# Kernel optimization log

Hardware: AMD Instinct MI355X
Metric: run time of the kernel (lower is better)

Reference implementation:

```python
import jax, jax.numpy as jnp
import numpy as np

# Module hyperparameters (init_kwargs)
N_CLASSES = 21
RADIUS = 5
SIZE = (256, 256)
SIGMA_DIST = 4.0
SIGMA_FEAT = 1.0
B, C = 8, 32


def _offsets(radius):
    """Integer (dy, dx) offsets with Euclidean distance < radius (includes (0,0))."""
    offs = []
    r = int(radius)
    for dy in range(-r + 1, r):
        for dx in range(-r + 1, r):
            if dy * dy + dx * dx < radius * radius:
                offs.append((dy, dx))
    return offs


OFFSETS = _offsets(RADIUS)  # 69 offsets for radius=5


def setup_inputs() -> dict:
    key = jax.random.key(0)
    k1, k2 = jax.random.split(key)
    H, W = SIZE
    classification = jax.random.uniform(k1, (B, N_CLASSES, H, W), dtype=jnp.float32)
    features = jax.random.normal(k2, (B, C, H, W), dtype=jnp.float32)
    return {"classification": classification, "features": features}


def reference(classification, features):
    # classification: [B, K, H, W] soft assignments S
    # features:       [B, C, H, W]
    Bb, K, H, W = classification.shape
    inv_sd2 = 1.0 / (SIGMA_DIST * SIGMA_DIST)
    inv_sf2 = 1.0 / (SIGMA_FEAT * SIGMA_FEAT)

    hs = jnp.arange(H)
    ws = jnp.arange(W)

    WS = jnp.zeros_like(classification)           # (W @ S), [B, K, H, W]
    degree = jnp.zeros((Bb, H, W), classification.dtype)

    # Loop over the small fixed set of neighbor offsets (69 for radius=5).
    for dy, dx in OFFSETS:
        f_nb = jnp.roll(features, (-dy, -dx), axis=(2, 3))
        s_nb = jnp.roll(classification, (-dy, -dx), axis=(2, 3))
        # mask out wrap-around: neighbor (h+dy, w+dx) must be in-bounds
        valid_h = (hs + dy >= 0) & (hs + dy < H)
        valid_w = (ws + dx >= 0) & (ws + dx < W)
        mask = (valid_h[:, None] & valid_w[None, :]).astype(classification.dtype)
        # Gaussian affinity: distance kernel * feature kernel
        feat_d2 = ((features - f_nb) ** 2).sum(axis=1)        # [B, H, W]
        w = jnp.exp(-(dy * dy + dx * dx) * inv_sd2 - feat_d2 * inv_sf2) * mask
        WS = WS + w[:, None] * s_nb
        degree = degree + w

    # numerator   = S^T W S : [B, K, K]
    # denominator = d^T S   : [B, K]
    num = jnp.einsum('bkhw,bjhw->bkj', classification, WS)
    den = jnp.einsum('bhw,bkhw->bk', degree, classification)
    return (num / den[:, None, :]).sum()
```

## Files before the change

kernel.cpp:

```cpp
#include <hip/hip_runtime.h>

#define HH 256
#define WW 256
#define HWPX 65536
#define BB 8
#define KK 21
#define CC 32

typedef _Float16 half2v __attribute__((ext_vector_type(2)));
union F4H { float4 f4; half2v h[4]; };

__global__ __launch_bounds__(256) void prep(const float* __restrict__ cls,
                                            const float* __restrict__ feat,
                                            float4* __restrict__ fpk,
                                            float2* __restrict__ TN) {
    const int tid = blockIdx.x * 256 + threadIdx.x;
    const int p4 = tid * 4;
    const int b = p4 >> 16;
    const int p = p4 & (HWPX - 1);

    const float* cbase = cls + (size_t)b * KK * HWPX + p;
    float4 s = make_float4(0.f, 0.f, 0.f, 0.f);
#pragma unroll
    for (int k = 0; k < KK; ++k) {
        float4 c = *(const float4*)(cbase + (size_t)k * HWPX);
        s.x += c.x; s.y += c.y; s.z += c.z; s.w += c.w;
    }

    const float* src = feat + (size_t)b * CC * HWPX + p;
    float nq[4] = {0.f, 0.f, 0.f, 0.f};
#pragma unroll
    for (int j = 0; j < 4; ++j) {
        float4 ch[8];
#pragma unroll
        for (int c = 0; c < 8; ++c)
            ch[c] = *(const float4*)(src + (size_t)(j * 8 + c) * HWPX);
#pragma unroll
        for (int px = 0; px < 4; ++px) {
            F4H u;
#pragma unroll
            for (int k = 0; k < 4; ++k) {
                float a  = ((const float*)&ch[2 * k])[px];
                float b2 = ((const float*)&ch[2 * k + 1])[px];
                u.h[k] = __builtin_bit_cast(half2v, __builtin_amdgcn_cvt_pkrtz(a, b2));
                nq[px] = __builtin_amdgcn_fdot2(u.h[k], u.h[k], nq[px], false);
            }
            fpk[(size_t)j * (BB * HWPX) + p4 + px] = u.f4;
        }
    }
    const float* sa = (const float*)&s;
#pragma unroll
    for (int px = 0; px < 4; ++px) TN[p4 + px] = make_float2(sa[px], nq[px]);
}

__global__ __launch_bounds__(256) void affinity4(const float4* __restrict__ fpk,
                                                 const float2* __restrict__ TN,
                                                 float* __restrict__ V,
                                                 float* __restrict__ deg) {
    const int L  = blockIdx.x;
    const int b  = L & 7;
    const int t  = L >> 3;
    const int by = t & 15;
    const int bx = t >> 4;
    const int lane = threadIdx.x & 63;
    const int wid  = threadIdx.x >> 6;
    const int gx  = bx * 64 + lane;
    const int gy0 = by * 16 + wid * 4;

    const size_t bofs = (size_t)b * HWPX;
    const float4* fb0 = fpk + bofs;
    const float4* fb1 = fpk + (size_t)1 * BB * HWPX + bofs;
    const float4* fb2 = fpk + (size_t)2 * BB * HWPX + bofs;
    const float4* fb3 = fpk + (size_t)3 * BB * HWPX + bofs;
    const float2* tnb = TN + bofs;

    F4H fp[4][4];
    float np_[4];
#pragma unroll
    for (int py = 0; py < 4; ++py) {
        const int pp = ((gy0 + py) << 8) | gx;
        fp[py][0].f4 = fb0[pp];
        fp[py][1].f4 = fb1[pp];
        fp[py][2].f4 = fb2[pp];
        fp[py][3].f4 = fb3[pp];
        np_[py] = tnb[pp].y;
    }

    float degacc[4] = {0.f, 0.f, 0.f, 0.f};
    float vacc[4]   = {0.f, 0.f, 0.f, 0.f};

#pragma unroll 1
    for (int dyi = 0; dyi < 12; ++dyi) {
        const int ny = gy0 + dyi - 4;
        if ((unsigned)ny >= HH) continue;
        const int rowq = ny << 8;

        int dy2[4];
        float base[4];
#pragma unroll
        for (int py = 0; py < 4; ++py) {
            const int d = dyi - 4 - py;
            dy2[py] = d * d;
            base[py] = fmaf(-0.03125f, (float)dy2[py], -0.5f * np_[py]);
        }
        const int mind = min(min(dy2[0], dy2[1]), min(dy2[2], dy2[3]));

#pragma unroll 3
        for (int dxi = 0; dxi < 9; ++dxi) {
            const int dx = dxi - 4;
            const int dx2 = dx * dx;
            if (mind + dx2 >= 25) continue;

            const int gx2 = gx + dx;
            const bool vx = (unsigned)gx2 < WW;
            const int q = rowq | min(max(gx2, 0), WW - 1);

            F4H nb0, nb1, nb2, nb3;
            nb0.f4 = fb0[q];
            nb1.f4 = fb1[q];
            nb2.f4 = fb2[q];
            nb3.f4 = fb3[q];
            const float2 tq = tnb[q];
            const float cdx = (float)dx2 * -0.03125f;

#pragma unroll
            for (int py = 0; py < 4; ++py) {
                if (dy2[py] + dx2 < 25) {
                    float acc = fmaf(-0.5f, tq.y, base[py] + cdx);
#pragma unroll
                    for (int k = 0; k < 4; ++k) {
                        acc = __builtin_amdgcn_fdot2(fp[py][0].h[k], nb0.h[k], acc, false);
                        acc = __builtin_amdgcn_fdot2(fp[py][1].h[k], nb1.h[k], acc, false);
                        acc = __builtin_amdgcn_fdot2(fp[py][2].h[k], nb2.h[k], acc, false);
                        acc = __builtin_amdgcn_fdot2(fp[py][3].h[k], nb3.h[k], acc, false);
                    }
                    float w = __builtin_exp2f(acc * 2.8853900817779268f);
                    w = vx ? w : 0.f;
                    degacc[py] += w;
                    vacc[py] = fmaf(w, tq.x, vacc[py]);
                }
            }
        }
    }

#pragma unroll
    for (int py = 0; py < 4; ++py) {
        const size_t o = bofs + ((size_t)(gy0 + py) << 8) + gx;
        V[o] = vacc[py];
        deg[o] = degacc[py];
    }
}

__global__ __launch_bounds__(256) void reduce_bj(const float* __restrict__ cls,
                                                 const float* __restrict__ V,
                                                 const float* __restrict__ deg,
                                                 float* __restrict__ numer,
                                                 float* __restrict__ denom) {
    __shared__ float smN[4][22], smD[4][22];
    const int b = blockIdx.y;
    const int p4 = (blockIdx.x * 256 + threadIdx.x) * 4;

    const float* clsb = cls + (size_t)b * KK * HWPX;
    const float4 v4 = *(const float4*)(V + (size_t)b * HWPX + p4);
    const float4 d4 = *(const float4*)(deg + (size_t)b * HWPX + p4);

    float accN[KK], accD[KK];
#pragma unroll
    for (int j = 0; j < KK; ++j) {
        float4 s4 = *(const float4*)(clsb + (size_t)j * HWPX + p4);
        float n = s4.x * v4.x;  n = fmaf(s4.y, v4.y, n);
        n = fmaf(s4.z, v4.z, n); n = fmaf(s4.w, v4.w, n);
        float d = s4.x * d4.x;  d = fmaf(s4.y, d4.y, d);
        d = fmaf(s4.z, d4.z, d); d = fmaf(s4.w, d4.w, d);
        accN[j] = n; accD[j] = d;
    }

    const int wid = threadIdx.x >> 6;
#pragma unroll
    for (int j = 0; j < KK; ++j) {
        float n = accN[j], d = accD[j];
#pragma unroll
        for (int off = 32; off > 0; off >>= 1) {
            n += __shfl_down(n, off);
            d += __shfl_down(d, off);
        }
        if ((threadIdx.x & 63) == 0) { smN[wid][j] = n; smD[wid][j] = d; }
    }
    __syncthreads();
    if (threadIdx.x < 2 * KK) {
        int half = threadIdx.x / KK;
        int j = threadIdx.x - half * KK;
        float acc = half ? (smD[0][j] + smD[1][j] + smD[2][j] + smD[3][j])
                         : (smN[0][j] + smN[1][j] + smN[2][j] + smN[3][j]);
        float* dst = half ? denom : numer;
        atomicAdd(&dst[b * KK + j], acc);
    }
}

__global__ __launch_bounds__(256) void finalize(const float* __restrict__ numer,
                                                const float* __restrict__ denom,
                                                float* __restrict__ out) {
    __shared__ float sm[4];
    int i = threadIdx.x;
    float r = 0.f;
    if (i < BB * KK) r = numer[i] / denom[i];
#pragma unroll
    for (int off = 32; off > 0; off >>= 1) r += __shfl_down(r, off);
    if ((i & 63) == 0) sm[i >> 6] = r;
    __syncthreads();
    if (i == 0) out[0] = sm[0] + sm[1] + sm[2] + sm[3];
}

extern "C" void kernel_launch(void* const* d_in, const int* in_sizes, int n_in,
                              void* d_out, int out_size, void* d_ws, size_t ws_size,
                              hipStream_t stream) {
    const float* cls  = (const float*)d_in[0];
    const float* feat = (const float*)d_in[1];
    float* out = (float*)d_out;

    const size_t BHW = (size_t)BB * HWPX;
    float4* fpk  = (float4*)d_ws;
    float2* TN   = (float2*)((char*)d_ws + BHW * 64);
    float*  V    = (float*)((char*)TN + BHW * 8);
    float*  deg  = V + BHW;
    float*  numer = deg + BHW;
    float*  denom = numer + BB * KK;

    (void)hipMemsetAsync(numer, 0, 2 * BB * KK * sizeof(float), stream);
    prep<<<dim3(BHW / 1024), dim3(256), 0, stream>>>(cls, feat, fpk, TN);
    affinity4<<<dim3(512), dim3(256), 0, stream>>>(fpk, TN, V, deg);
    reduce_bj<<<dim3(HWPX / 1024, BB), dim3(256), 0, stream>>>(cls, V, deg, numer, denom);
    finalize<<<dim3(1), dim3(256), 0, stream>>>(numer, denom, out);
}
```

Before: 205.9 us.

## Fuse per-class reduction into affinity kernel and halve pixels per prep thread

The affinity kernel now stages its per-pixel V and degree values in shared memory and immediately performs the class-weighted reduction with atomics. This removes the separate reduce kernel and the global round trip of V and degree. The prep kernel processes two pixels per thread instead of four and no longer unrolls the channel-group loop, which cuts register pressure and raises thread count. The cost is extra shared memory and a block-wide sync in the affinity kernel, plus classification reads now happening inside it.

```diff
diff --git a/kernel.cpp b/kernel.cpp
--- a/kernel.cpp
+++ b/kernel.cpp
@@ -15,48 +15,49 @@
                                             float4* __restrict__ fpk,
                                             float2* __restrict__ TN) {
     const int tid = blockIdx.x * 256 + threadIdx.x;
-    const int p4 = tid * 4;
-    const int b = p4 >> 16;
-    const int p = p4 & (HWPX - 1);
+    const int p2 = tid * 2;
+    const int b = p2 >> 16;
+    const int p = p2 & (HWPX - 1);
 
     const float* cbase = cls + (size_t)b * KK * HWPX + p;
-    float4 s = make_float4(0.f, 0.f, 0.f, 0.f);
+    float sx = 0.f, sy = 0.f;
 #pragma unroll
     for (int k = 0; k < KK; ++k) {
-        float4 c = *(const float4*)(cbase + (size_t)k * HWPX);
-        s.x += c.x; s.y += c.y; s.z += c.z; s.w += c.w;
+        float2 c = *(const float2*)(cbase + (size_t)k * HWPX);
+        sx += c.x; sy += c.y;
     }
 
     const float* src = feat + (size_t)b * CC * HWPX + p;
-    float nq[4] = {0.f, 0.f, 0.f, 0.f};
-#pragma unroll
+    float nq0 = 0.f, nq1 = 0.f;
+#pragma unroll 1
     for (int j = 0; j < 4; ++j) {
-        float4 ch[8];
+        float2 ch[8];
 #pragma unroll
         for (int c = 0; c < 8; ++c)
-            ch[c] = *(const float4*)(src + (size_t)(j * 8 + c) * HWPX);
-#pragma unroll
-        for (int px = 0; px < 4; ++px) {
-            F4H u;
-#pragma unroll
-            for (int k = 0; k < 4; ++k) {
-                float a  = ((const float*)&ch[2 * k])[px];
-                float b2 = ((const float*)&ch[2 * k + 1])[px];
-                u.h[k] = __builtin_bit_cast(half2v, __builtin_amdgcn_cvt_pkrtz(a, b2));
-                nq[px] = __builtin_amdgcn_fdot2(u.h[k], u.h[k], nq[px], false);
-            }
-            fpk[(size_t)j * (BB * HWPX) + p4 + px] = u.f4;
-        }
-    }
-    const float* sa = (const float*)&s;
-#pragma unroll
-    for (int px = 0; px < 4; ++px) TN[p4 + px] = make_float2(sa[px], nq[px]);
-}
-
-__global__ __launch_bounds__(256) void affinity4(const float4* __restrict__ fpk,
+            ch[c] = *(const float2*)(src + (size_t)(j * 8 + c) * HWPX);
+        F4H u0, u1;
+#pragma unroll
+        for (int k = 0; k < 4; ++k) {
+            u0.h[k] = __builtin_bit_cast(half2v, __builtin_amdgcn_cvt_pkrtz(ch[2 * k].x, ch[2 * k + 1].x));
+            nq0 = __builtin_amdgcn_fdot2(u0.h[k], u0.h[k], nq0, false);
+            u1.h[k] = __builtin_bit_cast(half2v, __builtin_amdgcn_cvt_pkrtz(ch[2 * k].y, ch[2 * k + 1].y));
+            nq1 = __builtin_amdgcn_fdot2(u1.h[k], u1.h[k], nq1, false);
+        }
+        fpk[(size_t)j * (BB * HWPX) + p2]     = u0.f4;
+        fpk[(size_t)j * (BB * HWPX) + p2 + 1] = u1.f4;
+    }
+    TN[p2]     = make_float2(sx, nq0);
+    TN[p2 + 1] = make_float2(sy, nq1);
+}
+
+__global__ __launch_bounds__(256) void affinity5(const float4* __restrict__ fpk,
                                                  const float2* __restrict__ TN,
-                                                 float* __restrict__ V,
-                                                 float* __restrict__ deg) {
+                                                 const float* __restrict__ cls,
+                                                 float* __restrict__ numer,
+                                                 float* __restrict__ denom) {
+    __shared__ float smV[1024], smD[1024];
+    __shared__ float pN[4][22], pD[4][22];
+
     const int L  = blockIdx.x;
     const int b  = L & 7;
     const int t  = L >> 3;
@@ -145,37 +146,31 @@
 
 #pragma unroll
     for (int py = 0; py < 4; ++py) {
-        const size_t o = bofs + ((size_t)(gy0 + py) << 8) + gx;
-        V[o] = vacc[py];
-        deg[o] = degacc[py];
-    }
-}
-
-__global__ __launch_bounds__(256) void reduce_bj(const float* __restrict__ cls,
-                                                 const float* __restrict__ V,
-                                                 const float* __restrict__ deg,
-                                                 float* __restrict__ numer,
-                                                 float* __restrict__ denom) {
-    __shared__ float smN[4][22], smD[4][22];
-    const int b = blockIdx.y;
-    const int p4 = (blockIdx.x * 256 + threadIdx.x) * 4;
-
-    const float* clsb = cls + (size_t)b * KK * HWPX;
-    const float4 v4 = *(const float4*)(V + (size_t)b * HWPX + p4);
-    const float4 d4 = *(const float4*)(deg + (size_t)b * HWPX + p4);
+        const int li = ((wid * 4 + py) << 6) | lane;
+        smV[li] = vacc[py];
+        smD[li] = degacc[py];
+    }
+    __syncthreads();
+
+    const int li0 = threadIdx.x * 4;
+    const int lr  = li0 >> 6;
+    const int lc  = li0 & 63;
+    const int gp  = ((by * 16 + lr) << 8) | (bx * 64 + lc);
+    const float4 v4 = *(const float4*)&smV[li0];
+    const float4 d4 = *(const float4*)&smD[li0];
+    const float* clsb = cls + (size_t)b * KK * HWPX + gp;
 
     float accN[KK], accD[KK];
-#pragma unroll
+#pragma unroll 7
     for (int j = 0; j < KK; ++j) {
-        float4 s4 = *(const float4*)(clsb + (size_t)j * HWPX + p4);
-        float n = s4.x * v4.x;  n = fmaf(s4.y, v4.y, n);
+        float4 s4 = *(const float4*)(clsb + (size_t)j * HWPX);
+        float n = s4.x * v4.x;   n = fmaf(s4.y, v4.y, n);
         n = fmaf(s4.z, v4.z, n); n = fmaf(s4.w, v4.w, n);
-        float d = s4.x * d4.x;  d = fmaf(s4.y, d4.y, d);
+        float d = s4.x * d4.x;   d = fmaf(s4.y, d4.y, d);
         d = fmaf(s4.z, d4.z, d); d = fmaf(s4.w, d4.w, d);
         accN[j] = n; accD[j] = d;
     }
 
-    const int wid = threadIdx.x >> 6;
 #pragma unroll
     for (int j = 0; j < KK; ++j) {
         float n = accN[j], d = accD[j];
@@ -184,14 +179,14 @@
             n += __shfl_down(n, off);
             d += __shfl_down(d, off);
         }
-        if ((threadIdx.x & 63) == 0) { smN[wid][j] = n; smD[wid][j] = d; }
+        if (lane == 0) { pN[wid][j] = n; pD[wid][j] = d; }
     }
     __syncthreads();
     if (threadIdx.x < 2 * KK) {
         int half = threadIdx.x / KK;
         int j = threadIdx.x - half * KK;
-        float acc = half ? (smD[0][j] + smD[1][j] + smD[2][j] + smD[3][j])
-                         : (smN[0][j] + smN[1][j] + smN[2][j] + smN[3][j]);
+        float acc = half ? (pD[0][j] + pD[1][j] + pD[2][j] + pD[3][j])
+                         : (pN[0][j] + pN[1][j] + pN[2][j] + pN[3][j]);
         float* dst = half ? denom : numer;
         atomicAdd(&dst[b * KK + j], acc);
     }
@@ -219,16 +214,13 @@
     float* out = (float*)d_out;
 
     const size_t BHW = (size_t)BB * HWPX;
-    float4* fpk  = (float4*)d_ws;
-    float2* TN   = (float2*)((char*)d_ws + BHW * 64);
-    float*  V    = (float*)((char*)TN + BHW * 8);
-    float*  deg  = V + BHW;
-    float*  numer = deg + BHW;
+    float4* fpk   = (float4*)d_ws;
+    float2* TN    = (float2*)((char*)d_ws + BHW * 64);
+    float*  numer = (float*)((char*)TN + BHW * 8);
     float*  denom = numer + BB * KK;
 
     (void)hipMemsetAsync(numer, 0, 2 * BB * KK * sizeof(float), stream);
-    prep<<<dim3(BHW / 1024), dim3(256), 0, stream>>>(cls, feat, fpk, TN);
-    affinity4<<<dim3(512), dim3(256), 0, stream>>>(fpk, TN, V, deg);
-    reduce_bj<<<dim3(HWPX / 1024, BB), dim3(256), 0, stream>>>(cls, V, deg, numer, denom);
+    prep<<<dim3(BHW / 512), dim3(256), 0, stream>>>(cls, feat, fpk, TN);
+    affinity5<<<dim3(512), dim3(256), 0, stream>>>(fpk, TN, cls, numer, denom);
     finalize<<<dim3(1), dim3(256), 0, stream>>>(numer, denom, out);
 }
```

Result: no change. 206.5 us (+0.3%).
